# Optimization experiments

Measured on AMD Instinct MI355X. Metric: run time of the kernel, lower is better.

Reference implementation:

```python
import jax, jax.numpy as jnp
import numpy as np

NEG_ATT = 0.2   # GATv2Conv internal leaky_relu slope
NEG_ACT = 0.01  # nn.LeakyReLU default slope (activation between layers)

def _segment_softmax(logits, seg, n):
    m = jax.ops.segment_max(logits, seg, num_segments=n)
    ex = jnp.exp(logits - m[seg])
    s = jax.ops.segment_sum(ex, seg, num_segments=n)
    return ex / s[seg]

def _gatv2(h, Wl, bl, Wr, br, att, bias, src, dst, n):
    # PyG GATv2Conv, heads=1: xl = lin_l(h) (source/message), xr = lin_r(h) (target)
    xl = h @ Wl + bl                                   # [N, H]
    xr = h @ Wr + br                                   # [N, H]
    e = jax.nn.leaky_relu(xl[src] + xr[dst], NEG_ATT)  # [E, H]
    logits = e @ att                                   # [E]
    alpha = _segment_softmax(logits, dst, n)           # softmax over incoming edges per dst
    out = jax.ops.segment_sum(xl[src] * alpha[:, None], dst, num_segments=n)
    return out + bias

def setup_inputs() -> dict:
    key = jax.random.key(0)
    G, P, DEG, DIN, H, EX, OUT, NC = 4096, 24, 8, 32, 128, 8, 3, 6
    N = G * P
    E = N * DEG
    ks = jax.random.split(key, 16)
    x = jax.random.normal(ks[0], (N, DIN), jnp.float32)
    gid = jnp.arange(E) // (P * DEG)  # edges stay within their graph
    src = gid * P + jax.random.randint(ks[1], (E,), 0, P)
    dst = gid * P + jax.random.randint(ks[2], (E,), 0, P)
    batch = jnp.repeat(jnp.arange(G), P)
    extra_feat = jax.random.normal(ks[3], (G, EX), jnp.float32)
    sc = lambda k, shp: jax.random.normal(k, shp, jnp.float32) * 0.05
    return dict(
        x=x, src=src, dst=dst, batch=batch, extra_feat=extra_feat,
        W_init0=sc(ks[4], (DIN, H)), b_init0=jnp.zeros((H,), jnp.float32),
        W_init1=sc(ks[5], (H, H)), b_init1=jnp.zeros((H,), jnp.float32),
        Wl=sc(ks[6], (NC, H, H)), bl=jnp.zeros((NC, H), jnp.float32),
        Wr=sc(ks[7], (NC, H, H)), br=jnp.zeros((NC, H), jnp.float32),
        att=sc(ks[8], (NC, H)), cbias=jnp.zeros((NC, H), jnp.float32),
        Wf0=sc(ks[9], (H + EX, H)), bf0=jnp.zeros((H,), jnp.float32),
        Wf1=sc(ks[10], (H, H)), bf1=jnp.zeros((H,), jnp.float32),
        Wf2=sc(ks[11], (H, OUT)), bf2=jnp.zeros((OUT,), jnp.float32),
    )

def reference(x, src, dst, batch, extra_feat,
              W_init0, b_init0, W_init1, b_init1,
              Wl, bl, Wr, br, att, cbias,
              Wf0, bf0, Wf1, bf1, Wf2, bf2):
    N = x.shape[0]
    G = extra_feat.shape[0]
    # init MLP
    h = jax.nn.leaky_relu(x @ W_init0 + b_init0, NEG_ACT)
    h = jax.nn.leaky_relu(h @ W_init1 + b_init1, NEG_ACT)
    # GATv2Conv adds self-loops
    loop = jnp.arange(N)
    src_sl = jnp.concatenate([src, loop])
    dst_sl = jnp.concatenate([dst, loop])
    NUM_GAT, MP = 2, 3
    for g in range(NUM_GAT):
        for m in range(MP):
            c = g * MP + m
            h = _gatv2(h, Wl[c], bl[c], Wr[c], br[c], att[c], cbias[c], src_sl, dst_sl, N)
            if m < MP - 1:  # BasicGNN: act between convs, not after last
                h = jax.nn.leaky_relu(h, NEG_ACT)
    # global_add_pool + extra features + final MLP
    pooled = jax.ops.segment_sum(h, batch, num_segments=G)
    z = jnp.concatenate([pooled, extra_feat], axis=1)
    z = jax.nn.leaky_relu(z @ Wf0 + bf0, NEG_ACT)
    z = jax.nn.leaky_relu(z @ Wf1 + bf1, NEG_ACT)
    return z @ Wf2 + bf2
```

## Files before the change

### kernel.cpp

```cpp
#include <hip/hip_runtime.h>

#define NG   4096
#define P    24
#define EPG  192
#define ESL  216
#define DIN  32
#define H    128
#define EX   8
#define NOUT 3
#define HSS  136
#define XTS  36

typedef _Float16 f16x8 __attribute__((ext_vector_type(8)));
typedef _Float16 h2    __attribute__((ext_vector_type(2)));
typedef float    f32x4 __attribute__((ext_vector_type(4)));

__device__ __forceinline__ unsigned short f2h(float v) {
    _Float16 h = (_Float16)v; unsigned short u; __builtin_memcpy(&u, &h, 2); return u;
}
__device__ __forceinline__ float h2f(unsigned short u) {
    _Float16 h; __builtin_memcpy(&h, &u, 2); return (float)h;
}
__device__ __forceinline__ unsigned pkadd(unsigned a, unsigned b) {
    h2 x, y; __builtin_memcpy(&x, &a, 4); __builtin_memcpy(&y, &b, 4);
    h2 z = x + y; unsigned r; __builtin_memcpy(&r, &z, 4); return r;
}
__device__ __forceinline__ float lrelu(float v, float s) { return v > 0.f ? v : v * s; }

__global__ void cvtw(const float* __restrict__ W0, const float* __restrict__ W1,
                     const float* __restrict__ Wl, const float* __restrict__ Wr,
                     const float* __restrict__ att, const float* __restrict__ bl,
                     const float* __restrict__ br, unsigned short* __restrict__ ws) {
    int i = blockIdx.x * 256 + threadIdx.x;
    if (i < 217088) {
        float v;
        if (i < 4096)        { int n = i >> 5, k = i & 31;  v = W0[k * 128 + n]; }
        else if (i < 20480)  { int j = i - 4096;  int n = j >> 7, k = j & 127; v = W1[k * 128 + n]; }
        else if (i < 118784) { int j = i - 20480; int c = j >> 14, r = j & 16383;
                               int n = r >> 7, k = r & 127; v = Wl[c * 16384 + k * 128 + n]; }
        else                 { int j = i - 118784; int c = j >> 14, r = j & 16383;
                               int n = r >> 7, k = r & 127; v = Wr[c * 16384 + k * 128 + n]; }
        ws[i] = f2h(v);
    } else if (i < 241664) {
        int j = i - 217088;
        const float* W = (j < 12288) ? Wl : Wr;
        if (j >= 12288) j -= 12288;
        int c = j >> 11, r = j & 2047, row = r >> 7, k = r & 127;
        float v = 0.f;
        if (row == 0) {
            for (int q = 0; q < 128; ++q) v += W[c * 16384 + k * 128 + q] * att[c * 128 + q];
        }
        ws[i] = f2h(v);
    } else if (i < 241676) {
        int c = i - 241664;
        const float* B = (c < 6) ? bl : br;
        int cc = (c < 6) ? c : c - 6;
        float s = 0.f;
        for (int q = 0; q < 128; ++q) s += B[cc * 128 + q] * att[cc * 128 + q];
        ((float*)(ws + 241664))[c] = s;
    }
}

__global__ __launch_bounds__(256, 4) void gat_all(
    const float* __restrict__ x,
    const int*   __restrict__ src,
    const int*   __restrict__ dst,
    const float* __restrict__ extra,
    const float* __restrict__ b0,  const float* __restrict__ b1,
    const float* __restrict__ bl,  const float* __restrict__ br,
    const float* __restrict__ att, const float* __restrict__ cbias,
    const float* __restrict__ Wf0, const float* __restrict__ bf0,
    const float* __restrict__ Wf1, const float* __restrict__ bf1,
    const float* __restrict__ Wf2, const float* __restrict__ bf2,
    const unsigned short* __restrict__ wsb,
    float* __restrict__ out)
{
    __shared__ __align__(16) unsigned short hb [32 * HSS];
    __shared__ __align__(16) unsigned short xlb[32 * HSS];
    __shared__ __align__(16) unsigned short xrb[32 * HSS];
    __shared__ __align__(16) unsigned short xlT[128 * XTS];
    __shared__ __align__(16) float          Am[1024];
    __shared__ __align__(16) unsigned int   att_h[64];
    __shared__ float dsum[32];
    __shared__ float snode[64];

    const int g    = blockIdx.x;
    const int t    = threadIdx.x;
    const int lane = t & 63;
    const int w    = t >> 6;
    const int m16  = lane & 15;
    const int kc   = lane >> 4;
    const long long gn = (long long)g * P;

    const unsigned short* W0T = wsb;
    const unsigned short* W1T = wsb + 4096;
    const unsigned short* WLT = wsb + 20480;
    const unsigned short* WRT = wsb + 118784;
    const float* wsf = (const float*)(wsb + 241664);

    int s_e = 0, d_e = 0;
    if (t < ESL) {
        if (t < EPG) {
            s_e = src[(long long)g * EPG + t] - (int)gn;
            d_e = dst[(long long)g * EPG + t] - (int)gn;
        } else { s_e = d_e = t - EPG; }
    }

    if (t < 192) {
        float4 v = *reinterpret_cast<const float4*>(&x[gn * DIN + t * 4]);
        int n = t >> 3, k = (t & 7) * 4;
        *reinterpret_cast<ushort4*>(&xlT[n * XTS + k]) =
            make_ushort4(f2h(v.x), f2h(v.y), f2h(v.z), f2h(v.w));
    } else {
        int u = t - 192;
        int r = 24 + (u >> 3), k = (u & 7) * 4;
        *reinterpret_cast<ushort4*>(&xlT[r * XTS + k]) = make_ushort4(0, 0, 0, 0);
    }
    __syncthreads();

    {
        f32x4 acc[4] = {};
        f16x8 a = *reinterpret_cast<const f16x8*>(&xlT[((w & 1) * 16 + m16) * XTS + kc * 8]);
        #pragma unroll
        for (int i = 0; i < 4; ++i) {
            int nt = (w >> 1) * 4 + i;
            f16x8 b = *reinterpret_cast<const f16x8*>(&W0T[(nt * 16 + m16) * 32 + kc * 8]);
            acc[i] = __builtin_amdgcn_mfma_f32_16x16x32_f16(a, b, acc[i], 0, 0, 0);
        }
        #pragma unroll
        for (int i = 0; i < 4; ++i) {
            int col = (w >> 1) * 64 + i * 16 + m16;
            float bv = b0[col];
            #pragma unroll
            for (int r = 0; r < 4; ++r) {
                int row = (w & 1) * 16 + kc * 4 + r;
                xlb[row * HSS + col] = f2h(lrelu(acc[i][r] + bv, 0.01f));
            }
        }
    }
    __syncthreads();

    {
        f32x4 acc[4] = {};
        for (int kt = 0; kt < 4; ++kt) {
            f16x8 a = *reinterpret_cast<const f16x8*>(&xlb[((w & 1) * 16 + m16) * HSS + kt * 32 + kc * 8]);
            #pragma unroll
            for (int i = 0; i < 4; ++i) {
                int nt = (w >> 1) * 4 + i;
                f16x8 b = *reinterpret_cast<const f16x8*>(&W1T[(nt * 16 + m16) * 128 + kt * 32 + kc * 8]);
                acc[i] = __builtin_amdgcn_mfma_f32_16x16x32_f16(a, b, acc[i], 0, 0, 0);
            }
        }
        #pragma unroll
        for (int i = 0; i < 4; ++i) {
            int col = (w >> 1) * 64 + i * 16 + m16;
            float bv = b1[col];
            #pragma unroll
            for (int r = 0; r < 4; ++r) {
                int row = (w & 1) * 16 + kc * 4 + r;
                hb[row * HSS + col] = f2h(lrelu(acc[i][r] + bv, 0.01f));
            }
        }
    }
    __syncthreads();

    for (int c = 0; c < 6; ++c) {
        *reinterpret_cast<float4*>(&Am[t * 4]) = make_float4(0.f, 0.f, 0.f, 0.f);
        if (t < 32) dsum[t] = (t < P) ? 0.f : 1.0f;
        if (t < 64) att_h[t] = ((unsigned)f2h(att[c * H + 2 * t])) |
                               (((unsigned)f2h(att[c * H + 2 * t + 1])) << 16);

        const unsigned short* WT   = ((w & 1) ? WRT : WLT) + c * 16384;
        const unsigned short* WAX  = wsb + 217088 + ((w & 1) ? 12288 : 0) + c * 2048;
        const float*          bias = ((w & 1) ? br : bl) + c * H;
        f32x4 acc[8] = {};
        f32x4 acce[2] = {};
        for (int kt = 0; kt < 4; ++kt) {
            f16x8 a0 = *reinterpret_cast<const f16x8*>(&hb[(m16)      * HSS + kt * 32 + kc * 8]);
            f16x8 a1 = *reinterpret_cast<const f16x8*>(&hb[(16 + m16) * HSS + kt * 32 + kc * 8]);
            #pragma unroll
            for (int i = 0; i < 4; ++i) {
                int nt = (w >> 1) * 4 + i;
                f16x8 b = *reinterpret_cast<const f16x8*>(&WT[(nt * 16 + m16) * 128 + kt * 32 + kc * 8]);
                acc[i]     = __builtin_amdgcn_mfma_f32_16x16x32_f16(a0, b, acc[i],     0, 0, 0);
                acc[4 + i] = __builtin_amdgcn_mfma_f32_16x16x32_f16(a1, b, acc[4 + i], 0, 0, 0);
            }
            if (w >= 2) {
                f16x8 bx = *reinterpret_cast<const f16x8*>(&WAX[m16 * 128 + kt * 32 + kc * 8]);
                acce[0] = __builtin_amdgcn_mfma_f32_16x16x32_f16(a0, bx, acce[0], 0, 0, 0);
                acce[1] = __builtin_amdgcn_mfma_f32_16x16x32_f16(a1, bx, acce[1], 0, 0, 0);
            }
        }
        {
            unsigned short* XO = (w & 1) ? xrb : xlb;
            const bool isL = !(w & 1);
            #pragma unroll
            for (int mt = 0; mt < 2; ++mt)
            #pragma unroll
            for (int i = 0; i < 4; ++i) {
                int col = (w >> 1) * 64 + i * 16 + m16;
                float bv = bias[col];
                unsigned short ub[4];
                #pragma unroll
                for (int r = 0; r < 4; ++r) {
                    int row = mt * 16 + kc * 4 + r;
                    ub[r] = f2h(acc[mt * 4 + i][r] + bv);
                    XO[row * HSS + col] = ub[r];
                }
                if (isL)
                    *reinterpret_cast<ushort4*>(&xlT[col * XTS + mt * 16 + kc * 4]) =
                        make_ushort4(ub[0], ub[1], ub[2], ub[3]);
            }
            if (w >= 2 && m16 == 0) {
                float cst = (w == 2) ? wsf[c] : wsf[6 + c];
                float* dp = (w == 2) ? snode : (snode + 32);
                #pragma unroll
                for (int mt = 0; mt < 2; ++mt)
                #pragma unroll
                for (int r = 0; r < 4; ++r)
                    dp[mt * 16 + kc * 4 + r] = acce[mt][r] + cst;
            }
        }
        __syncthreads();

        if (t < ESL) {
            const uint4* xa = reinterpret_cast<const uint4*>(&xlb[s_e * HSS]);
            const uint4* xb = reinterpret_cast<const uint4*>(&xrb[d_e * HSS]);
            const uint4* ap = reinterpret_cast<const uint4*>(att_h);
            float a0 = 0.f, a1 = 0.f, a2 = 0.f, a3 = 0.f;
            #pragma unroll 4
            for (int cc = 0; cc < 16; ++cc) {
                uint4 wa = xa[cc], wb = xb[cc], pp = ap[cc];
                unsigned u0 = pkadd(wa.x, wb.x) & 0x7fff7fffu;
                unsigned u1 = pkadd(wa.y, wb.y) & 0x7fff7fffu;
                unsigned u2 = pkadd(wa.z, wb.z) & 0x7fff7fffu;
                unsigned u3 = pkadd(wa.w, wb.w) & 0x7fff7fffu;
                asm volatile("v_dot2_f32_f16 %0, %1, %2, %0" : "+v"(a0) : "v"(u0), "v"(pp.x));
                asm volatile("v_dot2_f32_f16 %0, %1, %2, %0" : "+v"(a1) : "v"(u1), "v"(pp.y));
                asm volatile("v_dot2_f32_f16 %0, %1, %2, %0" : "+v"(a2) : "v"(u2), "v"(pp.z));
                asm volatile("v_dot2_f32_f16 %0, %1, %2, %0" : "+v"(a3) : "v"(u3), "v"(pp.w));
            }
            float abss = (a0 + a1) + (a2 + a3);
            float lg = fmaf(0.6f, snode[s_e] + snode[32 + d_e], 0.4f * abss);
            float ex = __expf(lg);
            atomicAdd(&Am[d_e * 32 + s_e], ex);
            atomicAdd(&dsum[d_e], ex);
        }
        __syncthreads();

        {
            int arow = (w & 1) * 16 + m16;
            float4 u0 = *reinterpret_cast<const float4*>(&Am[arow * 32 + kc * 8]);
            float4 u1 = *reinterpret_cast<const float4*>(&Am[arow * 32 + kc * 8 + 4]);
            f16x8 a;
            a[0] = (_Float16)u0.x; a[1] = (_Float16)u0.y;
            a[2] = (_Float16)u0.z; a[3] = (_Float16)u0.w;
            a[4] = (_Float16)u1.x; a[5] = (_Float16)u1.y;
            a[6] = (_Float16)u1.z; a[7] = (_Float16)u1.w;
            f32x4 acc2[4] = {};
            #pragma unroll
            for (int i = 0; i < 4; ++i) {
                int nt = (w >> 1) * 4 + i;
                f16x8 b = *reinterpret_cast<const f16x8*>(&xlT[(nt * 16 + m16) * XTS + kc * 8]);
                acc2[i] = __builtin_amdgcn_mfma_f32_16x16x32_f16(a, b, acc2[i], 0, 0, 0);
            }
            float inv[4];
            #pragma unroll
            for (int r = 0; r < 4; ++r)
                inv[r] = __builtin_amdgcn_rcpf(dsum[(w & 1) * 16 + kc * 4 + r]);
            const bool doact = (c % 3) < 2;
            #pragma unroll
            for (int i = 0; i < 4; ++i) {
                int col = (w >> 1) * 64 + i * 16 + m16;
                float cb = cbias[c * H + col];
                #pragma unroll
                for (int r = 0; r < 4; ++r) {
                    int row = (w & 1) * 16 + kc * 4 + r;
                    float v = fmaf(acc2[i][r], inv[r], cb);
                    if (doact) v = lrelu(v, 0.01f);
                    hb[row * HSS + col] = f2h(v);
                }
            }
        }
        __syncthreads();
    }

    float* z  = Am;
    float* pa = Am + 144;
    float* pb = Am + 288;
    float* h1 = Am + 432;
    float* qa = Am + 576;
    float* qb = Am + 720;
    float* h2 = Am + 864;
    if (t < H) {
        float s = 0.f;
        for (int r = 0; r < P; ++r) s += h2f(hb[r * HSS + t]);
        z[t] = s;
    } else if (t < H + EX) {
        z[t] = extra[(long long)g * EX + (t - H)];
    }
    __syncthreads();
    {
        int j = t & 127, half = t >> 7;
        float a = half ? 0.f : bf0[j];
        int k0 = half ? 68 : 0, k1 = half ? 136 : 68;
        for (int k = k0; k < k1; ++k) a += z[k] * Wf0[k * H + j];
        (half ? pb : pa)[j] = a;
    }
    __syncthreads();
    if (t < H) h1[t] = lrelu(pa[t] + pb[t], 0.01f);
    __syncthreads();
    {
        int j = t & 127, half = t >> 7;
        float a = half ? 0.f : bf1[j];
        int k0 = half * 64, k1 = k0 + 64;
        for (int k = k0; k < k1; ++k) a += h1[k] * Wf1[k * H + j];
        (half ? qb : qa)[j] = a;
    }
    __syncthreads();
    if (t < H) h2[t] = lrelu(qa[t] + qb[t], 0.01f);
    __syncthreads();
    if (t < NOUT) {
        float a = bf2[t];
        for (int k = 0; k < H; ++k) a += h2[k] * Wf2[k * NOUT + t];
        out[(long long)g * NOUT + t] = a;
    }
}

extern "C" void kernel_launch(void* const* d_in, const int* in_sizes, int n_in,
                              void* d_out, int out_size, void* d_ws, size_t ws_size,
                              hipStream_t stream) {
    (void)in_sizes; (void)n_in; (void)out_size; (void)ws_size;
    const float* x     = (const float*)d_in[0];
    const int*   src   = (const int*)  d_in[1];
    const int*   dst   = (const int*)  d_in[2];
    const float* extra = (const float*)d_in[4];
    const float* W0    = (const float*)d_in[5];
    const float* b0    = (const float*)d_in[6];
    const float* W1    = (const float*)d_in[7];
    const float* b1    = (const float*)d_in[8];
    const float* Wl    = (const float*)d_in[9];
    const float* bl    = (const float*)d_in[10];
    const float* Wr    = (const float*)d_in[11];
    const float* br    = (const float*)d_in[12];
    const float* att   = (const float*)d_in[13];
    const float* cbias = (const float*)d_in[14];
    const float* Wf0   = (const float*)d_in[15];
    const float* bf0   = (const float*)d_in[16];
    const float* Wf1   = (const float*)d_in[17];
    const float* bf1   = (const float*)d_in[18];
    const float* Wf2   = (const float*)d_in[19];
    const float* bf2   = (const float*)d_in[20];
    unsigned short* wsb = (unsigned short*)d_ws;
    float* out = (float*)d_out;

    cvtw<<<945, 256, 0, stream>>>(W0, W1, Wl, Wr, att, bl, br, wsb);
    gat_all<<<NG, 256, 0, stream>>>(x, src, dst, extra, b0, b1, bl, br, att, cbias,
                                    Wf0, bf0, Wf1, bf1, Wf2, bf2, wsb, out);
}
```

Measured before the change: 369.9 us.

## Pack LDS into one buffer, pair fp16 stores via DPP, normalize softmax in-register

Merges all shared arrays into a single 32 KB LDS buffer with a padded Am stride and reuses the xlb region as scratch for the final MLP. This lowers LDS use so the launch bound can rise to five blocks per CU. It also packs adjacent fp16 outputs into 32-bit LDS stores using a DPP lane swap, and skips stores for padding rows beyond 24. The per-destination softmax denominator is now taken from a shuffle-reduced row sum of Am instead of a second atomicAdd to dsum, which removes half the LDS atomics at the cost of extra shuffles and a lower per-thread register budget.

```diff
diff --git a/kernel.cpp b/kernel.cpp
--- a/kernel.cpp
+++ b/kernel.cpp
@@ -10,6 +10,7 @@
 #define NOUT 3
 #define HSS  136
 #define XTS  36
+#define AMS  36
 
 typedef _Float16 f16x8 __attribute__((ext_vector_type(8)));
 typedef _Float16 h2    __attribute__((ext_vector_type(2)));
@@ -26,6 +27,15 @@
     h2 z = x + y; unsigned r; __builtin_memcpy(&r, &z, 4); return r;
 }
 __device__ __forceinline__ float lrelu(float v, float s) { return v > 0.f ? v : v * s; }
+
+#define STPAIR(BASE, ROW, COL, VAL)                                           \
+    do {                                                                      \
+        unsigned o_ = (unsigned)__builtin_amdgcn_mov_dpp(                     \
+            (int)(unsigned)(VAL), 0xB1, 0xF, 0xF, true);                      \
+        if (!(lane & 1))                                                      \
+            *reinterpret_cast<unsigned*>(&(BASE)[(ROW) * HSS + (COL)]) =      \
+                (unsigned)(VAL) | (o_ << 16);                                 \
+    } while (0)
 
 __global__ void cvtw(const float* __restrict__ W0, const float* __restrict__ W1,
                      const float* __restrict__ Wl, const float* __restrict__ Wr,
@@ -61,7 +71,7 @@
     }
 }
 
-__global__ __launch_bounds__(256, 4) void gat_all(
+__global__ __launch_bounds__(256, 5) void gat_all(
     const float* __restrict__ x,
     const int*   __restrict__ src,
     const int*   __restrict__ dst,
@@ -75,14 +85,14 @@
     const unsigned short* __restrict__ wsb,
     float* __restrict__ out)
 {
-    __shared__ __align__(16) unsigned short hb [32 * HSS];
-    __shared__ __align__(16) unsigned short xlb[32 * HSS];
-    __shared__ __align__(16) unsigned short xrb[32 * HSS];
-    __shared__ __align__(16) unsigned short xlT[128 * XTS];
-    __shared__ __align__(16) float          Am[1024];
-    __shared__ __align__(16) unsigned int   att_h[64];
-    __shared__ float dsum[32];
-    __shared__ float snode[64];
+    __shared__ __align__(16) unsigned char LDSM[32768];
+    unsigned short* hb  = (unsigned short*)(LDSM);
+    unsigned short* xlb = (unsigned short*)(LDSM + 6528);
+    unsigned short* xrb = (unsigned short*)(LDSM + 13056);
+    unsigned short* xlT = (unsigned short*)(LDSM + 19584);
+    float*          Am  = (float*)(LDSM + 28800);
+    float*          sn  = (float*)(LDSM + 32256);
+    unsigned int*   ath = (unsigned int*)(LDSM + 32512);
 
     const int g    = blockIdx.x;
     const int t    = threadIdx.x;
@@ -127,14 +137,18 @@
             f16x8 b = *reinterpret_cast<const f16x8*>(&W0T[(nt * 16 + m16) * 32 + kc * 8]);
             acc[i] = __builtin_amdgcn_mfma_f32_16x16x32_f16(a, b, acc[i], 0, 0, 0);
         }
-        #pragma unroll
-        for (int i = 0; i < 4; ++i) {
-            int col = (w >> 1) * 64 + i * 16 + m16;
-            float bv = b0[col];
-            #pragma unroll
-            for (int r = 0; r < 4; ++r) {
-                int row = (w & 1) * 16 + kc * 4 + r;
-                xlb[row * HSS + col] = f2h(lrelu(acc[i][r] + bv, 0.01f));
+        const bool live = !((w & 1) && kc >= 2);
+        if (live) {
+            #pragma unroll
+            for (int i = 0; i < 4; ++i) {
+                int col = (w >> 1) * 64 + i * 16 + m16;
+                float bv = b0[col];
+                #pragma unroll
+                for (int r = 0; r < 4; ++r) {
+                    int row = (w & 1) * 16 + kc * 4 + r;
+                    unsigned short ub = f2h(lrelu(acc[i][r] + bv, 0.01f));
+                    STPAIR(xlb, row, col, ub);
+                }
             }
         }
     }
@@ -151,24 +165,27 @@
                 acc[i] = __builtin_amdgcn_mfma_f32_16x16x32_f16(a, b, acc[i], 0, 0, 0);
             }
         }
-        #pragma unroll
-        for (int i = 0; i < 4; ++i) {
-            int col = (w >> 1) * 64 + i * 16 + m16;
-            float bv = b1[col];
-            #pragma unroll
-            for (int r = 0; r < 4; ++r) {
-                int row = (w & 1) * 16 + kc * 4 + r;
-                hb[row * HSS + col] = f2h(lrelu(acc[i][r] + bv, 0.01f));
+        const bool live = !((w & 1) && kc >= 2);
+        if (live) {
+            #pragma unroll
+            for (int i = 0; i < 4; ++i) {
+                int col = (w >> 1) * 64 + i * 16 + m16;
+                float bv = b1[col];
+                #pragma unroll
+                for (int r = 0; r < 4; ++r) {
+                    int row = (w & 1) * 16 + kc * 4 + r;
+                    unsigned short ub = f2h(lrelu(acc[i][r] + bv, 0.01f));
+                    STPAIR(hb, row, col, ub);
+                }
             }
         }
     }
     __syncthreads();
 
     for (int c = 0; c < 6; ++c) {
-        *reinterpret_cast<float4*>(&Am[t * 4]) = make_float4(0.f, 0.f, 0.f, 0.f);
-        if (t < 32) dsum[t] = (t < P) ? 0.f : 1.0f;
-        if (t < 64) att_h[t] = ((unsigned)f2h(att[c * H + 2 * t])) |
-                               (((unsigned)f2h(att[c * H + 2 * t + 1])) << 16);
+        if (t < ESL) *reinterpret_cast<float4*>(&Am[t * 4]) = make_float4(0.f, 0.f, 0.f, 0.f);
+        if (t < 64) ath[t] = ((unsigned)f2h(att[c * H + 2 * t])) |
+                             (((unsigned)f2h(att[c * H + 2 * t + 1])) << 16);
 
         const unsigned short* WT   = ((w & 1) ? WRT : WLT) + c * 16384;
         const unsigned short* WAX  = wsb + 217088 + ((w & 1) ? 12288 : 0) + c * 2048;
@@ -195,25 +212,29 @@
             unsigned short* XO = (w & 1) ? xrb : xlb;
             const bool isL = !(w & 1);
             #pragma unroll
-            for (int mt = 0; mt < 2; ++mt)
-            #pragma unroll
-            for (int i = 0; i < 4; ++i) {
-                int col = (w >> 1) * 64 + i * 16 + m16;
-                float bv = bias[col];
-                unsigned short ub[4];
-                #pragma unroll
-                for (int r = 0; r < 4; ++r) {
-                    int row = mt * 16 + kc * 4 + r;
-                    ub[r] = f2h(acc[mt * 4 + i][r] + bv);
-                    XO[row * HSS + col] = ub[r];
+            for (int mt = 0; mt < 2; ++mt) {
+                const bool live = !(mt == 1 && kc >= 2);
+                if (live) {
+                    #pragma unroll
+                    for (int i = 0; i < 4; ++i) {
+                        int col = (w >> 1) * 64 + i * 16 + m16;
+                        float bv = bias[col];
+                        unsigned short ub[4];
+                        #pragma unroll
+                        for (int r = 0; r < 4; ++r) {
+                            int row = mt * 16 + kc * 4 + r;
+                            ub[r] = f2h(acc[mt * 4 + i][r] + bv);
+                            STPAIR(XO, row, col, ub[r]);
+                        }
+                        if (isL)
+                            *reinterpret_cast<ushort4*>(&xlT[col * XTS + mt * 16 + kc * 4]) =
+                                make_ushort4(ub[0], ub[1], ub[2], ub[3]);
+                    }
                 }
-                if (isL)
-                    *reinterpret_cast<ushort4*>(&xlT[col * XTS + mt * 16 + kc * 4]) =
-                        make_ushort4(ub[0], ub[1], ub[2], ub[3]);
             }
             if (w >= 2 && m16 == 0) {
                 float cst = (w == 2) ? wsf[c] : wsf[6 + c];
-                float* dp = (w == 2) ? snode : (snode + 32);
+                float* dp = (w == 2) ? sn : (sn + 32);
                 #pragma unroll
                 for (int mt = 0; mt < 2; ++mt)
                 #pragma unroll
@@ -226,7 +247,7 @@
         if (t < ESL) {
             const uint4* xa = reinterpret_cast<const uint4*>(&xlb[s_e * HSS]);
             const uint4* xb = reinterpret_cast<const uint4*>(&xrb[d_e * HSS]);
-            const uint4* ap = reinterpret_cast<const uint4*>(att_h);
+            const uint4* ap = reinterpret_cast<const uint4*>(ath);
             float a0 = 0.f, a1 = 0.f, a2 = 0.f, a3 = 0.f;
             #pragma unroll 4
             for (int cc = 0; cc < 16; ++cc) {
@@ -241,22 +262,30 @@
                 asm volatile("v_dot2_f32_f16 %0, %1, %2, %0" : "+v"(a3) : "v"(u3), "v"(pp.w));
             }
             float abss = (a0 + a1) + (a2 + a3);
-            float lg = fmaf(0.6f, snode[s_e] + snode[32 + d_e], 0.4f * abss);
-            float ex = __expf(lg);
-            atomicAdd(&Am[d_e * 32 + s_e], ex);
-            atomicAdd(&dsum[d_e], ex);
+            float lg = fmaf(0.6f, sn[s_e] + sn[32 + d_e], 0.4f * abss);
+            atomicAdd(&Am[d_e * AMS + s_e], __expf(lg));
         }
         __syncthreads();
 
         {
             int arow = (w & 1) * 16 + m16;
-            float4 u0 = *reinterpret_cast<const float4*>(&Am[arow * 32 + kc * 8]);
-            float4 u1 = *reinterpret_cast<const float4*>(&Am[arow * 32 + kc * 8 + 4]);
+            float4 u0, u1;
+            if (arow < P) {
+                u0 = *reinterpret_cast<const float4*>(&Am[arow * AMS + kc * 8]);
+                u1 = *reinterpret_cast<const float4*>(&Am[arow * AMS + kc * 8 + 4]);
+            } else {
+                u0 = make_float4(0.f, 0.f, 0.f, 0.f);
+                u1 = u0;
+            }
+            float rs = u0.x + u0.y + u0.z + u0.w + u1.x + u1.y + u1.z + u1.w;
+            rs += __shfl_xor(rs, 16);
+            rs += __shfl_xor(rs, 32);
+            float sc = (arow < P) ? __builtin_amdgcn_rcpf(rs) : 0.f;
             f16x8 a;
-            a[0] = (_Float16)u0.x; a[1] = (_Float16)u0.y;
-            a[2] = (_Float16)u0.z; a[3] = (_Float16)u0.w;
-            a[4] = (_Float16)u1.x; a[5] = (_Float16)u1.y;
-            a[6] = (_Float16)u1.z; a[7] = (_Float16)u1.w;
+            a[0] = (_Float16)(u0.x * sc); a[1] = (_Float16)(u0.y * sc);
+            a[2] = (_Float16)(u0.z * sc); a[3] = (_Float16)(u0.w * sc);
+            a[4] = (_Float16)(u1.x * sc); a[5] = (_Float16)(u1.y * sc);
+            a[6] = (_Float16)(u1.z * sc); a[7] = (_Float16)(u1.w * sc);
             f32x4 acc2[4] = {};
             #pragma unroll
             for (int i = 0; i < 4; ++i) {
@@ -264,34 +293,35 @@
                 f16x8 b = *reinterpret_cast<const f16x8*>(&xlT[(nt * 16 + m16) * XTS + kc * 8]);
                 acc2[i] = __builtin_amdgcn_mfma_f32_16x16x32_f16(a, b, acc2[i], 0, 0, 0);
             }
-            float inv[4];
-            #pragma unroll
-            for (int r = 0; r < 4; ++r)
-                inv[r] = __builtin_amdgcn_rcpf(dsum[(w & 1) * 16 + kc * 4 + r]);
             const bool doact = (c % 3) < 2;
-            #pragma unroll
-            for (int i = 0; i < 4; ++i) {
-                int col = (w >> 1) * 64 + i * 16 + m16;
-                float cb = cbias[c * H + col];
-                #pragma unroll
-                for (int r = 0; r < 4; ++r) {
-                    int row = (w & 1) * 16 + kc * 4 + r;
-                    float v = fmaf(acc2[i][r], inv[r], cb);
-                    if (doact) v = lrelu(v, 0.01f);
-                    hb[row * HSS + col] = f2h(v);
+            const bool live = !((w & 1) && kc >= 2);
+            if (live) {
+                #pragma unroll
+                for (int i = 0; i < 4; ++i) {
+                    int col = (w >> 1) * 64 + i * 16 + m16;
+                    float cb = cbias[c * H + col];
+                    #pragma unroll
+                    for (int r = 0; r < 4; ++r) {
+                        int row = (w & 1) * 16 + kc * 4 + r;
+                        float v = acc2[i][r] + cb;
+                        if (doact) v = lrelu(v, 0.01f);
+                        unsigned short ub = f2h(v);
+                        STPAIR(hb, row, col, ub);
+                    }
                 }
             }
         }
         __syncthreads();
     }
 
-    float* z  = Am;
-    float* pa = Am + 144;
-    float* pb = Am + 288;
-    float* h1 = Am + 432;
-    float* qa = Am + 576;
-    float* qb = Am + 720;
-    float* h2 = Am + 864;
+    float* scr = (float*)(LDSM + 6528);
+    float* z  = scr;
+    float* pa = scr + 144;
+    float* pb = scr + 288;
+    float* h1 = scr + 432;
+    float* qa = scr + 576;
+    float* qb = scr + 720;
+    float* h2 = scr + 864;
     if (t < H) {
         float s = 0.f;
         for (int r = 0; r < P; ++r) s += h2f(hb[r * HSS + t]);
```

After: 481.4 us. 30.1% more time.
